# Optimization experiments

Hardware: AMD Instinct MI355X
Metric: run time of the kernel (lower is better)

## Reference

```python
import jax, jax.numpy as jnp
import numpy as np

B, N, H, W = 128, 8192, 7, 7


def setup_inputs() -> dict:
    key = jax.random.key(0)
    ks = jax.random.split(key, 10)
    inp = {
        'x': jax.random.normal(ks[0], (B, N, H, W), dtype=jnp.float32),
        'y': jax.random.normal(ks[1], (B, N), dtype=jnp.float32),
        # nn.MultiheadAttention(embed_dim=1, num_heads=1) params (all scalar)
        'wq': jax.random.normal(ks[2], (), dtype=jnp.float32),
        'wk': jax.random.normal(ks[3], (), dtype=jnp.float32),
        'wv': jax.random.normal(ks[4], (), dtype=jnp.float32),
        'bq': jax.random.normal(ks[5], (), dtype=jnp.float32) * 0.1,
        'bk': jax.random.normal(ks[6], (), dtype=jnp.float32) * 0.1,
        'bv': jax.random.normal(ks[7], (), dtype=jnp.float32) * 0.1,
        'wo': jax.random.normal(ks[8], (), dtype=jnp.float32),
        'bo': jax.random.normal(ks[9], (), dtype=jnp.float32) * 0.1,
    }
    return inp


def _mha1(q_src, kv_src, wq, bq, wk, bk, wv, bv, wo, bo):
    # embed_dim=1, num_heads=1, scale = 1/sqrt(1) = 1.
    # torch sees (seq=B, batch=N, embed=1): attention mixes the B axis per n.
    q = q_src * wq + bq            # [B, N]
    k = kv_src * wk + bk           # [B, N]
    v = kv_src * wv + bv           # [B, N]
    scores = jnp.einsum('in,jn->ijn', q, k)      # [B, B, N]
    a = jax.nn.softmax(scores, axis=1)           # softmax over keys j
    out = jnp.einsum('ijn,jn->in', a, v)         # [B, N]
    return out * wo + bo


def reference(x, y, wq, bq, wk, bk, wv, bv, wo, bo):
    xp = jnp.mean(x, axis=(2, 3))                # AdaptiveAvgPool2d((1,1)) -> [B, N]
    self_x = _mha1(xp, xp, wq, bq, wk, bk, wv, bv, wo, bo)
    self_y = _mha1(y, y, wq, bq, wk, bk, wv, bv, wo, bo)
    cross_x = _mha1(xp, y, wq, bq, wk, bk, wv, bv, wo, bo)
    cross_y = _mha1(y, xp, wq, bq, wk, bk, wv, bv, wo, bo)
    f_x = xp + self_x
    f_y = y + self_y
    c_f_x = cross_x + f_x
    c_f_y = cross_y + f_y
    return jnp.concatenate((c_f_x, c_f_y), axis=1)   # [B, 2N]
```

## Files before the change

### kernel.cpp

```cpp
#include <hip/hip_runtime.h>


constexpr int B_SEQ = 128;
constexpr int N_COL = 8192;
constexpr int HWP   = 49;
constexpr int NT    = 256;
constexpr int TC    = 4;

__global__ __launch_bounds__(NT, 6) void rsca_fused(
    const float* __restrict__ x, const float* __restrict__ y,
    const float* __restrict__ pwq, const float* __restrict__ pwk,
    const float* __restrict__ pwv, const float* __restrict__ pbq,
    const float* __restrict__ pbk, const float* __restrict__ pbv,
    const float* __restrict__ pwo, const float* __restrict__ pbo,
    float* __restrict__ out)
{
    __shared__ float2 kvxT[TC][B_SEQ];
    __shared__ float2 kvyT[TC][B_SEQ];
    __shared__ float  pmn[2][TC][8], pmx[2][TC][8];
    __shared__ float  klmn[2][TC], klmx[2][TC];

    const int t  = threadIdx.x;
    const int n0 = blockIdx.x * TC;

    const float wq = pwq[0], wk = pwk[0], wv = pwv[0];
    const float bq = pbq[0], bk = pbk[0], bv = pbv[0];
    const float wo = pwo[0], bo = pbo[0];
    const float L2E = 1.4426950408889634f;
    const float wkL = wk * L2E, bkL = bk * L2E;
    const float alpha = wo * wv;
    const float beta2 = 2.0f * (wo * bv + bo);

    for (int cell = t; cell < B_SEQ * TC; cell += NT) {
        const int j = cell >> 2, c = cell & 3;
        const float fy = y[(size_t)j * N_COL + n0 + c];
        kvyT[c][j] = make_float2(fmaf(fy, wkL, bkL), fy);
    }

    const int ql  = t & 3;
    const int seg = t >> 2;
    for (int pass = 0; pass < 2; ++pass) {
        const int j = pass * 64 + seg;
        const float4* __restrict__ base =
            (const float4*)(x + ((size_t)j * N_COL + n0) * (size_t)HWP);
        float4 v[13];
        #pragma unroll
        for (int k = 0; k < 12; ++k) v[k] = base[ql + 4 * k];
        v[12] = base[48];

        float s0 = 0.f, s1 = 0.f, s2 = 0.f, s3 = 0.f;
        s0 += v[0].x + v[0].y + v[0].z + v[0].w;
        s0 += v[1].x + v[1].y + v[1].z + v[1].w;
        s0 += v[2].x + v[2].y + v[2].z + v[2].w;
        s1 += v[4].x + v[4].y + v[4].z + v[4].w;
        s1 += v[5].x + v[5].y + v[5].z + v[5].w;
        s2 += v[7].x + v[7].y + v[7].z + v[7].w;
        s2 += v[8].x + v[8].y + v[8].z + v[8].w;
        s3 += v[10].x + v[10].y + v[10].z + v[10].w;
        s3 += v[11].x + v[11].y + v[11].z + v[11].w;
        { const float sm = v[3].x + v[3].y + v[3].z + v[3].w;
          const float cr = (ql == 0) ? v[3].x : 0.0f;
          s0 += cr; s1 += sm - cr; }
        { const float sm = v[6].x + v[6].y + v[6].z + v[6].w;
          const float cr = (ql == 0) ? (v[6].x + v[6].y) : 0.0f;
          s1 += cr; s2 += sm - cr; }
        { const float sm = v[9].x + v[9].y + v[9].z + v[9].w;
          const float cr = (ql == 0) ? (v[9].x + v[9].y + v[9].z) : 0.0f;
          s2 += cr; s3 += sm - cr; }
        const float tail = v[12].x + v[12].y + v[12].z + v[12].w;

        s0 += __shfl_xor(s0, 1); s1 += __shfl_xor(s1, 1);
        s2 += __shfl_xor(s2, 1); s3 += __shfl_xor(s3, 1);
        s0 += __shfl_xor(s0, 2); s1 += __shfl_xor(s1, 2);
        s2 += __shfl_xor(s2, 2); s3 += __shfl_xor(s3, 2);
        float r = s0;
        r = (ql == 1) ? s1 : r;
        r = (ql == 2) ? s2 : r;
        r = (ql == 3) ? (s3 + tail) : r;
        const float mean = r * (1.0f / HWP);
        kvxT[ql][j] = make_float2(fmaf(mean, wkL, bkL), mean);
    }
    __syncthreads();

    if (t < 64) {
        const int set = t >> 5, c = (t >> 3) & 3, part = t & 7;
        float mn = 3.4e38f, mx = -3.4e38f;
        #pragma unroll
        for (int k = 0; k < 16; ++k) {
            const int j = part * 16 + k;
            const float vv = set ? kvyT[c][j].x : kvxT[c][j].x;
            mn = fminf(mn, vv);
            mx = fmaxf(mx, vv);
        }
        pmn[set][c][part] = mn;
        pmx[set][c][part] = mx;
    }
    __syncthreads();
    if (t < 8) {
        const int set = t >> 2, c = t & 3;
        float mn = 3.4e38f, mx = -3.4e38f;
        #pragma unroll
        for (int k = 0; k < 8; ++k) {
            mn = fminf(mn, pmn[set][c][k]);
            mx = fmaxf(mx, pmx[set][c][k]);
        }
        klmn[set][c] = mn;
        klmx[set][c] = mx;
    }
    __syncthreads();

    const int i  = t & (B_SEQ - 1);
    const int ch = t >> 7;
    #pragma unroll
    for (int cc = 0; cc < 2; ++cc) {
        const int c = ch * 2 + cc;
        const float2* __restrict__ px = kvxT[c];
        const float2* __restrict__ py = kvyT[c];
        const float xi = px[i].y;
        const float yi = py[i].y;
        const float qx = fmaf(xi, wq, bq);
        const float qy = fmaf(yi, wq, bq);
        const float nmsx = -(qx >= 0.0f ? qx * klmx[0][c] : qx * klmn[0][c]);
        const float nmcy = -(qy >= 0.0f ? qy * klmx[0][c] : qy * klmn[0][c]);
        const float nmsy = -(qy >= 0.0f ? qy * klmx[1][c] : qy * klmn[1][c]);
        const float nmcx = -(qx >= 0.0f ? qx * klmx[1][c] : qx * klmn[1][c]);

        float s0sx = 0.f, s1sx = 0.f, s0cy = 0.f, s1cy = 0.f;
        float s0sy = 0.f, s1sy = 0.f, s0cx = 0.f, s1cx = 0.f;
        for (int j0 = 0; j0 < B_SEQ; j0 += 8) {
            float2 kx[8], ky[8];
            #pragma unroll
            for (int jj = 0; jj < 8; ++jj) kx[jj] = px[j0 + jj];
            #pragma unroll
            for (int jj = 0; jj < 8; ++jj) ky[jj] = py[j0 + jj];
            #pragma unroll
            for (int jj = 0; jj < 8; ++jj) {
                const float e1 = __builtin_amdgcn_exp2f(fmaf(qx, kx[jj].x, nmsx));
                const float e2 = __builtin_amdgcn_exp2f(fmaf(qy, kx[jj].x, nmcy));
                const float e3 = __builtin_amdgcn_exp2f(fmaf(qy, ky[jj].x, nmsy));
                const float e4 = __builtin_amdgcn_exp2f(fmaf(qx, ky[jj].x, nmcx));
                s1sx = fmaf(e1, kx[jj].y, s1sx); s0sx += e1;
                s1cy = fmaf(e2, kx[jj].y, s1cy); s0cy += e2;
                s1sy = fmaf(e3, ky[jj].y, s1sy); s0sy += e3;
                s1cx = fmaf(e4, ky[jj].y, s1cx); s0cx += e4;
            }
        }
        const float mx_attn = s1sx * __builtin_amdgcn_rcpf(s0sx)
                            + s1cx * __builtin_amdgcn_rcpf(s0cx);
        const float my_attn = s1sy * __builtin_amdgcn_rcpf(s0sy)
                            + s1cy * __builtin_amdgcn_rcpf(s0cy);
        out[(size_t)i * (2 * N_COL) + n0 + c]         = fmaf(alpha, mx_attn, beta2 + xi);
        out[(size_t)i * (2 * N_COL) + N_COL + n0 + c] = fmaf(alpha, my_attn, beta2 + yi);
    }
}

extern "C" void kernel_launch(void* const* d_in, const int* in_sizes, int n_in,
                              void* d_out, int out_size, void* d_ws, size_t ws_size,
                              hipStream_t stream) {
    const float* x   = (const float*)d_in[0];
    const float* y   = (const float*)d_in[1];
    const float* pwq = (const float*)d_in[2];
    const float* pwk = (const float*)d_in[3];
    const float* pwv = (const float*)d_in[4];
    const float* pbq = (const float*)d_in[5];
    const float* pbk = (const float*)d_in[6];
    const float* pbv = (const float*)d_in[7];
    const float* pwo = (const float*)d_in[8];
    const float* pbo = (const float*)d_in[9];
    float* out = (float*)d_out;

    rsca_fused<<<dim3(N_COL / TC), dim3(NT), 0, stream>>>(
        x, y, pwq, pwk, pwv, pbq, pbk, pbv, pwo, pbo, out);
}
```

Before: 332.8 us.

## Process 16 columns per block with double-buffered prefetch overlapping attention

Each block now handles four groups of four columns. The x/y loads and pooling for the next group are issued while the current group's attention runs, using double-buffered shared staging. Key min/max is now computed with wave shuffles, keys are derived on the fly from the raw values, and the inner loop uses packed v2f FMAs. Outputs are staged in shared memory and written as float4 rows. The trade-offs are fewer blocks (512) at lower occupancy (launch bounds 2) and higher register pressure from holding prefetched vectors during attention.

After: 326.5 us. About the same (-1.9%).

```diff
diff --git a/kernel.cpp b/kernel.cpp
--- a/kernel.cpp
+++ b/kernel.cpp
@@ -6,8 +6,22 @@
 constexpr int HWP   = 49;
 constexpr int NT    = 256;
 constexpr int TC    = 4;
-
-__global__ __launch_bounds__(NT, 6) void rsca_fused(
+constexpr int G     = 4;
+constexpr int CPB   = TC * G;
+constexpr int VSTR  = 132;
+constexpr int OSTR  = 21;
+
+typedef float v2f __attribute__((ext_vector_type(2)));
+
+#if __has_builtin(__builtin_elementwise_fma)
+#define VFMA(a, b, c) __builtin_elementwise_fma((a), (b), (c))
+#else
+__device__ __forceinline__ v2f VFMA(v2f a, v2f b, v2f c) {
+    v2f r; r.x = fmaf(a.x, b.x, c.x); r.y = fmaf(a.y, b.y, c.y); return r;
+}
+#endif
+
+__global__ __launch_bounds__(NT, 2) void rsca_fused(
     const float* __restrict__ x, const float* __restrict__ y,
     const float* __restrict__ pwq, const float* __restrict__ pwk,
     const float* __restrict__ pwv, const float* __restrict__ pbq,
@@ -15,13 +29,18 @@
     const float* __restrict__ pwo, const float* __restrict__ pbo,
     float* __restrict__ out)
 {
-    __shared__ float2 kvxT[TC][B_SEQ];
-    __shared__ float2 kvyT[TC][B_SEQ];
-    __shared__ float  pmn[2][TC][8], pmx[2][TC][8];
-    __shared__ float  klmn[2][TC], klmx[2][TC];
-
-    const int t  = threadIdx.x;
-    const int n0 = blockIdx.x * TC;
+    __shared__ float vls[2][2][TC * VSTR];
+    __shared__ float pmn[2][2][8][TC];
+    __shared__ float pmx[2][2][8][TC];
+    __shared__ float obuf[2][B_SEQ * OSTR];
+
+    const int t       = threadIdx.x;
+    const int bid     = blockIdx.x;
+    const int colbase = bid * CPB;
+    const int ql      = t & 3;
+    const int seg     = t >> 2;
+    const int lane    = t & 63;
+    const int wid     = t >> 6;
 
     const float wq = pwq[0], wk = pwk[0], wv = pwv[0];
     const float bq = pbq[0], bk = pbk[0], bv = pbv[0];
@@ -31,23 +50,16 @@
     const float alpha = wo * wv;
     const float beta2 = 2.0f * (wo * bv + bo);
 
-    for (int cell = t; cell < B_SEQ * TC; cell += NT) {
-        const int j = cell >> 2, c = cell & 3;
-        const float fy = y[(size_t)j * N_COL + n0 + c];
-        kvyT[c][j] = make_float2(fmaf(fy, wkL, bkL), fy);
-    }
-
-    const int ql  = t & 3;
-    const int seg = t >> 2;
-    for (int pass = 0; pass < 2; ++pass) {
-        const int j = pass * 64 + seg;
+    auto issue_pass = [&](int g, int p, float4 (&v)[13]) {
+        const int j = p * 64 + seg;
         const float4* __restrict__ base =
-            (const float4*)(x + ((size_t)j * N_COL + n0) * (size_t)HWP);
-        float4 v[13];
+            (const float4*)(x + ((size_t)j * N_COL + colbase + g * TC) * (size_t)HWP);
         #pragma unroll
         for (int k = 0; k < 12; ++k) v[k] = base[ql + 4 * k];
         v[12] = base[48];
-
+    };
+
+    auto reduce_pass = [&](int p, int nb, const float4 (&v)[13]) {
         float s0 = 0.f, s1 = 0.f, s2 = 0.f, s3 = 0.f;
         s0 += v[0].x + v[0].y + v[0].z + v[0].w;
         s0 += v[1].x + v[1].y + v[1].z + v[1].w;
@@ -68,7 +80,6 @@
           const float cr = (ql == 0) ? (v[9].x + v[9].y + v[9].z) : 0.0f;
           s2 += cr; s3 += sm - cr; }
         const float tail = v[12].x + v[12].y + v[12].z + v[12].w;
-
         s0 += __shfl_xor(s0, 1); s1 += __shfl_xor(s1, 1);
         s2 += __shfl_xor(s2, 1); s3 += __shfl_xor(s3, 1);
         s0 += __shfl_xor(s0, 2); s1 += __shfl_xor(s1, 2);
@@ -78,79 +89,167 @@
         r = (ql == 2) ? s2 : r;
         r = (ql == 3) ? (s3 + tail) : r;
         const float mean = r * (1.0f / HWP);
-        kvxT[ql][j] = make_float2(fmaf(mean, wkL, bkL), mean);
+        const int j = p * 64 + seg;
+        vls[nb][0][ql * VSTR + j] = mean;
+        float mn = mean, mx = mean;
+        #pragma unroll
+        for (int off = 4; off <= 32; off <<= 1) {
+            mn = fminf(mn, __shfl_xor(mn, off));
+            mx = fmaxf(mx, __shfl_xor(mx, off));
+        }
+        if (lane < 4) {
+            pmn[nb][0][p * 4 + wid][ql] = mn;
+            pmx[nb][0][p * 4 + wid][ql] = mx;
+        }
+    };
+
+    auto stage_y = [&](int nb, float fy0, float fy1) {
+        vls[nb][1][ql * VSTR + seg]      = fy0;
+        vls[nb][1][ql * VSTR + seg + 64] = fy1;
+        float mn = fminf(fy0, fy1), mx = fmaxf(fy0, fy1);
+        #pragma unroll
+        for (int off = 4; off <= 32; off <<= 1) {
+            mn = fminf(mn, __shfl_xor(mn, off));
+            mx = fmaxf(mx, __shfl_xor(mx, off));
+        }
+        if (lane < 4) {
+            pmn[nb][1][wid][ql] = mn;
+            pmx[nb][1][wid][ql] = mx;
+        }
+    };
+
+    const int ch = t >> 7;
+    const int i  = t & (B_SEQ - 1);
+
+    auto attn = [&](int g, int cb, int cc) {
+        const int c = ch * 2 + cc;
+        const float* __restrict__ vx = &vls[cb][0][c * VSTR];
+        const float* __restrict__ vy = &vls[cb][1][c * VSTR];
+
+        float vxmn = pmn[cb][0][0][c], vxmx = pmx[cb][0][0][c];
+        #pragma unroll
+        for (int s = 1; s < 8; ++s) {
+            vxmn = fminf(vxmn, pmn[cb][0][s][c]);
+            vxmx = fmaxf(vxmx, pmx[cb][0][s][c]);
+        }
+        float vymn = pmn[cb][1][0][c], vymx = pmx[cb][1][0][c];
+        #pragma unroll
+        for (int s = 1; s < 4; ++s) {
+            vymn = fminf(vymn, pmn[cb][1][s][c]);
+            vymx = fmaxf(vymx, pmx[cb][1][s][c]);
+        }
+        const float axv = fmaf(vxmx, wkL, bkL), bxv = fmaf(vxmn, wkL, bkL);
+        const float kxmx = fmaxf(axv, bxv), kxmn = fminf(axv, bxv);
+        const float ayv = fmaf(vymx, wkL, bkL), byv = fmaf(vymn, wkL, bkL);
+        const float kymx = fmaxf(ayv, byv), kymn = fminf(ayv, byv);
+
+        const float xi = vx[i], yi = vy[i];
+        const float qx = fmaf(xi, wq, bq), qy = fmaf(yi, wq, bq);
+        const float nmsx = -(qx >= 0.f ? qx * kxmx : qx * kxmn);
+        const float nmcy = -(qy >= 0.f ? qy * kxmx : qy * kxmn);
+        const float nmsy = -(qy >= 0.f ? qy * kymx : qy * kymn);
+        const float nmcx = -(qx >= 0.f ? qx * kymx : qx * kymn);
+
+        const float qxw = qx * wkL, qyw = qy * wkL;
+        const v2f qxw2 = {qxw, qxw}, qyw2 = {qyw, qyw};
+        const float csx = fmaf(qx, bkL, nmsx), ccy = fmaf(qy, bkL, nmcy);
+        const float csy = fmaf(qy, bkL, nmsy), ccx = fmaf(qx, bkL, nmcx);
+        const v2f csx2 = {csx, csx}, ccy2 = {ccy, ccy};
+        const v2f csy2 = {csy, csy}, ccx2 = {ccx, ccx};
+
+        v2f s0sx = {0.f, 0.f}, s1sx = {0.f, 0.f};
+        v2f s0cy = {0.f, 0.f}, s1cy = {0.f, 0.f};
+        v2f s0sy = {0.f, 0.f}, s1sy = {0.f, 0.f};
+        v2f s0cx = {0.f, 0.f}, s1cx = {0.f, 0.f};
+
+        for (int j0 = 0; j0 < B_SEQ; j0 += 8) {
+            const float4 a0 = *(const float4*)&vx[j0];
+            const float4 a1 = *(const float4*)&vx[j0 + 4];
+            const float4 b0 = *(const float4*)&vy[j0];
+            const float4 b1 = *(const float4*)&vy[j0 + 4];
+            auto px2 = [&](float v0, float v1) {
+                const v2f vv = {v0, v1};
+                v2f t1 = VFMA(qxw2, vv, csx2);
+                v2f e1; e1.x = __builtin_amdgcn_exp2f(t1.x);
+                        e1.y = __builtin_amdgcn_exp2f(t1.y);
+                s1sx = VFMA(e1, vv, s1sx); s0sx += e1;
+                v2f t2 = VFMA(qyw2, vv, ccy2);
+                v2f e2; e2.x = __builtin_amdgcn_exp2f(t2.x);
+                        e2.y = __builtin_amdgcn_exp2f(t2.y);
+                s1cy = VFMA(e2, vv, s1cy); s0cy += e2;
+            };
+            auto py2 = [&](float v0, float v1) {
+                const v2f vv = {v0, v1};
+                v2f t3 = VFMA(qyw2, vv, csy2);
+                v2f e3; e3.x = __builtin_amdgcn_exp2f(t3.x);
+                        e3.y = __builtin_amdgcn_exp2f(t3.y);
+                s1sy = VFMA(e3, vv, s1sy); s0sy += e3;
+                v2f t4 = VFMA(qxw2, vv, ccx2);
+                v2f e4; e4.x = __builtin_amdgcn_exp2f(t4.x);
+                        e4.y = __builtin_amdgcn_exp2f(t4.y);
+                s1cx = VFMA(e4, vv, s1cx); s0cx += e4;
+            };
+            px2(a0.x, a0.y); px2(a0.z, a0.w); px2(a1.x, a1.y); px2(a1.z, a1.w);
+            py2(b0.x, b0.y); py2(b0.z, b0.w); py2(b1.x, b1.y); py2(b1.z, b1.w);
+        }
+        const float S0sx = s0sx.x + s0sx.y, S1sx = s1sx.x + s1sx.y;
+        const float S0cy = s0cy.x + s0cy.y, S1cy = s1cy.x + s1cy.y;
+        const float S0sy = s0sy.x + s0sy.y, S1sy = s1sy.x + s1sy.y;
+        const float S0cx = s0cx.x + s0cx.y, S1cx = s1cx.x + s1cx.y;
+        const float mx_attn = S1sx * __builtin_amdgcn_rcpf(S0sx)
+                            + S1cx * __builtin_amdgcn_rcpf(S0cx);
+        const float my_attn = S1sy * __builtin_amdgcn_rcpf(S0sy)
+                            + S1cy * __builtin_amdgcn_rcpf(S0cy);
+        obuf[0][i * OSTR + g * TC + c] = fmaf(alpha, mx_attn, beta2 + xi);
+        obuf[1][i * OSTR + g * TC + c] = fmaf(alpha, my_attn, beta2 + yi);
+    };
+
+    float4 va[13], vb[13];
+    float fy0, fy1;
+    {
+        const int col = colbase + ql;
+        issue_pass(0, 0, va);
+        issue_pass(0, 1, vb);
+        fy0 = y[(size_t)seg * N_COL + col];
+        fy1 = y[(size_t)(seg + 64) * N_COL + col];
+        reduce_pass(0, 0, va);
+        stage_y(0, fy0, fy1);
+        reduce_pass(1, 0, vb);
     }
     __syncthreads();
 
-    if (t < 64) {
-        const int set = t >> 5, c = (t >> 3) & 3, part = t & 7;
-        float mn = 3.4e38f, mx = -3.4e38f;
-        #pragma unroll
-        for (int k = 0; k < 16; ++k) {
-            const int j = part * 16 + k;
-            const float vv = set ? kvyT[c][j].x : kvxT[c][j].x;
-            mn = fminf(mn, vv);
-            mx = fmaxf(mx, vv);
-        }
-        pmn[set][c][part] = mn;
-        pmx[set][c][part] = mx;
+    int cur = 0;
+    for (int g = 0; g < G; ++g) {
+        const int nb = cur ^ 1;
+        const bool pf = (g + 1 < G);
+        if (pf) {
+            const int col = colbase + (g + 1) * TC + ql;
+            issue_pass(g + 1, 0, va);
+            fy0 = y[(size_t)seg * N_COL + col];
+            fy1 = y[(size_t)(seg + 64) * N_COL + col];
+        }
+        attn(g, cur, 0);
+        if (pf) {
+            reduce_pass(0, nb, va);
+            stage_y(nb, fy0, fy1);
+            issue_pass(g + 1, 1, vb);
+        }
+        attn(g, cur, 1);
+        if (pf) reduce_pass(1, nb, vb);
+        __syncthreads();
+        cur = nb;
     }
-    __syncthreads();
-    if (t < 8) {
-        const int set = t >> 2, c = t & 3;
-        float mn = 3.4e38f, mx = -3.4e38f;
-        #pragma unroll
-        for (int k = 0; k < 8; ++k) {
-            mn = fminf(mn, pmn[set][c][k]);
-            mx = fmaxf(mx, pmx[set][c][k]);
-        }
-        klmn[set][c] = mn;
-        klmx[set][c] = mx;
-    }
-    __syncthreads();
-
-    const int i  = t & (B_SEQ - 1);
-    const int ch = t >> 7;
+
     #pragma unroll
-    for (int cc = 0; cc < 2; ++cc) {
-        const int c = ch * 2 + cc;
-        const float2* __restrict__ px = kvxT[c];
-        const float2* __restrict__ py = kvyT[c];
-        const float xi = px[i].y;
-        const float yi = py[i].y;
-        const float qx = fmaf(xi, wq, bq);
-        const float qy = fmaf(yi, wq, bq);
-        const float nmsx = -(qx >= 0.0f ? qx * klmx[0][c] : qx * klmn[0][c]);
-        const float nmcy = -(qy >= 0.0f ? qy * klmx[0][c] : qy * klmn[0][c]);
-        const float nmsy = -(qy >= 0.0f ? qy * klmx[1][c] : qy * klmn[1][c]);
-        const float nmcx = -(qx >= 0.0f ? qx * klmx[1][c] : qx * klmn[1][c]);
-
-        float s0sx = 0.f, s1sx = 0.f, s0cy = 0.f, s1cy = 0.f;
-        float s0sy = 0.f, s1sy = 0.f, s0cx = 0.f, s1cx = 0.f;
-        for (int j0 = 0; j0 < B_SEQ; j0 += 8) {
-            float2 kx[8], ky[8];
-            #pragma unroll
-            for (int jj = 0; jj < 8; ++jj) kx[jj] = px[j0 + jj];
-            #pragma unroll
-            for (int jj = 0; jj < 8; ++jj) ky[jj] = py[j0 + jj];
-            #pragma unroll
-            for (int jj = 0; jj < 8; ++jj) {
-                const float e1 = __builtin_amdgcn_exp2f(fmaf(qx, kx[jj].x, nmsx));
-                const float e2 = __builtin_amdgcn_exp2f(fmaf(qy, kx[jj].x, nmcy));
-                const float e3 = __builtin_amdgcn_exp2f(fmaf(qy, ky[jj].x, nmsy));
-                const float e4 = __builtin_amdgcn_exp2f(fmaf(qx, ky[jj].x, nmcx));
-                s1sx = fmaf(e1, kx[jj].y, s1sx); s0sx += e1;
-                s1cy = fmaf(e2, kx[jj].y, s1cy); s0cy += e2;
-                s1sy = fmaf(e3, ky[jj].y, s1sy); s0sy += e3;
-                s1cx = fmaf(e4, ky[jj].y, s1cx); s0cx += e4;
-            }
-        }
-        const float mx_attn = s1sx * __builtin_amdgcn_rcpf(s0sx)
-                            + s1cx * __builtin_amdgcn_rcpf(s0cx);
-        const float my_attn = s1sy * __builtin_amdgcn_rcpf(s0sy)
-                            + s1cy * __builtin_amdgcn_rcpf(s0cy);
-        out[(size_t)i * (2 * N_COL) + n0 + c]         = fmaf(alpha, mx_attn, beta2 + xi);
-        out[(size_t)i * (2 * N_COL) + N_COL + n0 + c] = fmaf(alpha, my_attn, beta2 + yi);
+    for (int idx = t; idx < 2 * B_SEQ * TC; idx += NT) {
+        const int set = idx >> 9;
+        const int rem = idx & 511;
+        const int ii  = rem >> 2;
+        const int q   = rem & 3;
+        const float* p = &obuf[set][ii * OSTR + q * 4];
+        float4 val;
+        val.x = p[0]; val.y = p[1]; val.z = p[2]; val.w = p[3];
+        *(float4*)&out[(size_t)ii * (2 * N_COL) + (size_t)set * N_COL + colbase + q * 4] = val;
     }
 }
 
@@ -169,6 +268,6 @@
     const float* pbo = (const float*)d_in[9];
     float* out = (float*)d_out;
 
-    rsca_fused<<<dim3(N_COL / TC), dim3(NT), 0, stream>>>(
+    rsca_fused<<<dim3(N_COL / CPB), dim3(NT), 0, stream>>>(
         x, y, pwq, pwk, pwv, pbq, pbk, pbv, pwo, pbo, out);
 }
```
